# Kernel tuning notes

Hardware: AMD Instinct MI355X
Metric: run time of the kernel (lower is better)

## Reference

```python
import jax, jax.numpy as jnp
import numpy as np

N = 50000      # nodes
E = 800000     # edges (before self-loops)
IN = 128       # in_channels
HID = 64       # hidden_channels
HEADS = 4      # num_heads of gat1
ACT = 5        # num_actions
NEG_SLOPE = 0.2


def gat_conv(x, edge_index, W, a_src, a_dst, bias, heads, out_ch):
    """PyG-style GATConv (concat=True, add_self_loops=True, eval mode)."""
    n = x.shape[0]
    loops = jnp.arange(n)
    src = jnp.concatenate([edge_index[0], loops])  # messages flow src -> dst
    dst = jnp.concatenate([edge_index[1], loops])
    h = (x @ W).reshape(n, heads, out_ch)                 # [N,H,C]
    alpha_src = jnp.sum(h * a_src, axis=-1)               # [N,H]
    alpha_dst = jnp.sum(h * a_dst, axis=-1)               # [N,H]
    e = jax.nn.leaky_relu(alpha_src[src] + alpha_dst[dst], NEG_SLOPE)  # [Et,H]
    # numerically-stable segment softmax over incoming edges of each dst node
    e_max = jax.lax.stop_gradient(jax.ops.segment_max(e, dst, num_segments=n))
    e_max = jnp.where(jnp.isfinite(e_max), e_max, 0.0)
    p = jnp.exp(e - e_max[dst])                           # [Et,H]
    denom = jax.ops.segment_sum(p, dst, num_segments=n)   # [N,H]
    alpha = p / (denom[dst] + 1e-16)                      # [Et,H]
    out = jax.ops.segment_sum(h[src] * alpha[:, :, None], dst, num_segments=n)
    return out.reshape(n, heads * out_ch) + bias


def setup_inputs() -> dict:
    key = jax.random.key(0)
    ks = jax.random.split(key, 12)
    s = 0.1
    return {
        "x": jax.random.normal(ks[0], (N, IN), jnp.float32),
        "edge_index": jax.random.randint(ks[1], (2, E), 0, N, dtype=jnp.int32),
        "W1": jax.random.normal(ks[2], (IN, HEADS * HID), jnp.float32) * s,
        "a1_src": jax.random.normal(ks[3], (HEADS, HID), jnp.float32) * s,
        "a1_dst": jax.random.normal(ks[4], (HEADS, HID), jnp.float32) * s,
        "b1": jnp.zeros((HEADS * HID,), jnp.float32),
        "W2": jax.random.normal(ks[5], (HEADS * HID, HID), jnp.float32) * s,
        "a2_src": jax.random.normal(ks[6], (1, HID), jnp.float32) * s,
        "a2_dst": jax.random.normal(ks[7], (1, HID), jnp.float32) * s,
        "b2": jnp.zeros((HID,), jnp.float32),
        "Wfc": jax.random.normal(ks[8], (HID, ACT), jnp.float32) * s,
        "bfc": jnp.zeros((ACT,), jnp.float32),
    }


def reference(x, edge_index, W1, a1_src, a1_dst, b1, W2, a2_src, a2_dst, b2, Wfc, bfc):
    # x.view(-1, F) is a no-op for already-flat [N, F] input; dropout skipped (eval).
    h = jax.nn.relu(gat_conv(x, edge_index, W1, a1_src, a1_dst, b1, HEADS, HID))
    h = jax.nn.relu(gat_conv(h, edge_index, W2, a2_src, a2_dst, b2, 1, HID))
    return h @ Wfc + bfc  # [N, num_actions]
```

## Files before the change

### kernel.cpp

```cpp
#include <hip/hip_runtime.h>

#define NEG_SLOPE 0.2f

__device__ __forceinline__ float leaky(float x) { return x > 0.f ? x : NEG_SLOPE * x; }

__global__ void k_count(const int* __restrict__ dst, int E, int* __restrict__ cnt) {
    int i = blockIdx.x * blockDim.x + threadIdx.x;
    if (i < E) atomicAdd(&cnt[dst[i]], 1);
}

__global__ __launch_bounds__(256) void k_scanA(const int* __restrict__ cnt, int* __restrict__ rowptr,
                                               int* __restrict__ bsum, int n) {
    int b = blockIdx.x, t = threadIdx.x;
    int lane = t & 63, w = t >> 6;
    int i0 = b * 1024 + t * 4;
    int v0 = (i0 + 0 < n) ? cnt[i0 + 0] : 0;
    int v1 = (i0 + 1 < n) ? cnt[i0 + 1] : 0;
    int v2 = (i0 + 2 < n) ? cnt[i0 + 2] : 0;
    int v3 = (i0 + 3 < n) ? cnt[i0 + 3] : 0;
    int r0 = v0, r1 = r0 + v1, r2 = r1 + v2, r3 = r2 + v3;
    int s = r3;
    int q = s;
    #pragma unroll
    for (int off = 1; off < 64; off <<= 1) {
        int tval = __shfl_up(q, off);
        if (lane >= off) q += tval;
    }
    __shared__ int wsum[4];
    if (lane == 63) wsum[w] = q;
    __syncthreads();
    int woff = 0;
    #pragma unroll
    for (int k = 0; k < 4; k++) if (k < w) woff += wsum[k];
    int excl = woff + q - s;
    if (i0 + 0 < n) rowptr[1 + i0 + 0] = excl + r0;
    if (i0 + 1 < n) rowptr[1 + i0 + 1] = excl + r1;
    if (i0 + 2 < n) rowptr[1 + i0 + 2] = excl + r2;
    if (i0 + 3 < n) rowptr[1 + i0 + 3] = excl + r3;
    if (t == 255) bsum[b] = woff + q;
}

__global__ void k_scanB(const int* __restrict__ bsum, int* __restrict__ bscan, int nb) {
    int lane = threadIdx.x & 63;
    int v = (lane < nb) ? bsum[lane] : 0;
    #pragma unroll
    for (int off = 1; off < 64; off <<= 1) {
        int t = __shfl_up(v, off);
        if (lane >= off) v += t;
    }
    if (lane < nb) bscan[lane] = v;
}

__global__ __launch_bounds__(256) void k_scanC(int* __restrict__ rowptr, const int* __restrict__ bscan, int n) {
    int b = blockIdx.x, t = threadIdx.x;
    int i0 = b * 1024 + t * 4;
    if (b == 0) {
        if (t == 0) rowptr[0] = 0;
        return;
    }
    int add = bscan[b - 1];
    #pragma unroll
    for (int j = 0; j < 4; j++)
        if (i0 + j < n) rowptr[1 + i0 + j] += add;
}

__global__ void k_copy(const int* __restrict__ src, int* __restrict__ dst, int n) {
    int i = blockIdx.x * blockDim.x + threadIdx.x;
    if (i < n) dst[i] = src[i];
}

__global__ void k_scatter(const int* __restrict__ srcn, const int* __restrict__ dstn, int E,
                          int* __restrict__ wptr, int* __restrict__ col) {
    int i = blockIdx.x * blockDim.x + threadIdx.x;
    if (i < E) {
        int d = dstn[i];
        int pos = atomicAdd(&wptr[d], 1);
        col[pos] = srcn[i];
    }
}

template <int BMT>
__global__ __launch_bounds__(256) void k_gemm(const float* __restrict__ A, const float* __restrict__ B,
                                              float* __restrict__ C, int M, int N, int K) {
    constexpr int RT = BMT / 16;
    constexpr int APASS = BMT / 32;
    __shared__ float As[32][BMT + 4];
    __shared__ float Bs[32][68];
    int row0 = blockIdx.x * BMT, col0 = blockIdx.y * 64;
    int tid = threadIdx.x;
    int tx = tid & 15, ty = tid >> 4;
    float acc[RT][4] = {};
    for (int kk = 0; kk < K; kk += 32) {
        int ar = tid >> 3;
        int ac = (tid & 7) * 4;
        #pragma unroll
        for (int p = 0; p < APASS; p++) {
            int r = ar + p * 32;
            int gr = row0 + r;
            float4 v = make_float4(0.f, 0.f, 0.f, 0.f);
            if (gr < M) v = *reinterpret_cast<const float4*>(&A[(size_t)gr * K + kk + ac]);
            As[ac + 0][r] = v.x; As[ac + 1][r] = v.y;
            As[ac + 2][r] = v.z; As[ac + 3][r] = v.w;
        }
        int br = tid >> 4;
        int bc = (tid & 15) * 4;
        #pragma unroll
        for (int p = 0; p < 2; p++) {
            int r = br + p * 16;
            float4 v = *reinterpret_cast<const float4*>(&B[(size_t)(kk + r) * N + col0 + bc]);
            *reinterpret_cast<float4*>(&Bs[r][bc]) = v;
        }
        __syncthreads();
        #pragma unroll
        for (int k = 0; k < 32; k++) {
            float a[RT];
            #pragma unroll
            for (int i = 0; i < RT; i += 4) {
                float4 av = *reinterpret_cast<const float4*>(&As[k][ty * RT + i]);
                a[i + 0] = av.x; a[i + 1] = av.y; a[i + 2] = av.z; a[i + 3] = av.w;
            }
            float4 bv = *reinterpret_cast<const float4*>(&Bs[k][tx * 4]);
            float b[4] = {bv.x, bv.y, bv.z, bv.w};
            #pragma unroll
            for (int i = 0; i < RT; i++)
                #pragma unroll
                for (int j = 0; j < 4; j++) acc[i][j] = fmaf(a[i], b[j], acc[i][j]);
        }
        __syncthreads();
    }
    #pragma unroll
    for (int i = 0; i < RT; i++) {
        int gr = row0 + ty * RT + i;
        if (gr < M) {
            float4 v = make_float4(acc[i][0], acc[i][1], acc[i][2], acc[i][3]);
            *reinterpret_cast<float4*>(&C[(size_t)gr * N + col0 + tx * 4]) = v;
        }
    }
}

__global__ __launch_bounds__(256) void k_alpha1(const float* __restrict__ h,
                                                const float* __restrict__ a_s, const float* __restrict__ a_d,
                                                float* __restrict__ asrc, float* __restrict__ adst, int n) {
    int node = blockIdx.x;
    int t = threadIdx.x, hd = t >> 6, lane = t & 63;
    float v = h[(size_t)node * 256 + t];
    float ps = v * a_s[t], pd = v * a_d[t];
    #pragma unroll
    for (int off = 32; off; off >>= 1) { ps += __shfl_xor(ps, off); pd += __shfl_xor(pd, off); }
    if (lane == 0) { asrc[node * 4 + hd] = ps; adst[node * 4 + hd] = pd; }
}

__global__ __launch_bounds__(256) void k_alpha2(const float* __restrict__ h,
                                                const float* __restrict__ a_s, const float* __restrict__ a_d,
                                                float* __restrict__ asrc, float* __restrict__ adst, int n) {
    int node = blockIdx.x * 4 + (threadIdx.x >> 6);
    int lane = threadIdx.x & 63;
    if (node >= n) return;
    float v = h[(size_t)node * 64 + lane];
    float ps = v * a_s[lane], pd = v * a_d[lane];
    #pragma unroll
    for (int off = 32; off; off >>= 1) { ps += __shfl_xor(ps, off); pd += __shfl_xor(pd, off); }
    if (lane == 0) { asrc[node] = ps; adst[node] = pd; }
}

__global__ __launch_bounds__(256) void k_agg1(const float* __restrict__ h, const float* __restrict__ asrc,
                                              const float* __restrict__ adst, const int* __restrict__ rowptr,
                                              const int* __restrict__ col, const float* __restrict__ bias,
                                              float* __restrict__ out, int n) {
    int node = blockIdx.x;
    int t = threadIdx.x, hd = t >> 6, l = t & 63;
    int rep = l >> 4, q = l & 15;
    int base = rowptr[node], deg = rowptr[node + 1] - base;
    float adst_n = adst[node * 4 + hd];
    float e_self = leaky(asrc[node * 4 + hd] + adst_n);
    float m = e_self;
    for (int i = l; i < deg; i += 64) {
        int s = col[base + i];
        m = fmaxf(m, leaky(asrc[s * 4 + hd] + adst_n));
    }
    #pragma unroll
    for (int off = 32; off; off >>= 1) m = fmaxf(m, __shfl_xor(m, off));

    float p_self = __expf(e_self - m);
    float4 acc = make_float4(0.f, 0.f, 0.f, 0.f);
    if (rep == 0) {
        float4 hv = *reinterpret_cast<const float4*>(&h[(size_t)node * 256 + hd * 64 + q * 4]);
        acc.x = p_self * hv.x; acc.y = p_self * hv.y; acc.z = p_self * hv.z; acc.w = p_self * hv.w;
    }
    float dsum = (l == 0) ? p_self : 0.f;

    for (int c0 = 0; c0 < deg; c0 += 8) {
        int ia = c0 + rep, ib = ia + 4;
        bool va = ia < deg, vb = ib < deg;
        int sa = 0, sb = 0;
        if (va) sa = col[base + ia];
        if (vb) sb = col[base + ib];
        float4 ha = make_float4(0.f, 0.f, 0.f, 0.f), hb = ha;
        if (va) ha = *reinterpret_cast<const float4*>(&h[(size_t)sa * 256 + hd * 64 + q * 4]);
        if (vb) hb = *reinterpret_cast<const float4*>(&h[(size_t)sb * 256 + hd * 64 + q * 4]);
        float pa = 0.f, pb = 0.f;
        if (va) pa = __expf(leaky(asrc[sa * 4 + hd] + adst_n) - m);
        if (vb) pb = __expf(leaky(asrc[sb * 4 + hd] + adst_n) - m);
        acc.x = fmaf(pa, ha.x, acc.x); acc.y = fmaf(pa, ha.y, acc.y);
        acc.z = fmaf(pa, ha.z, acc.z); acc.w = fmaf(pa, ha.w, acc.w);
        acc.x = fmaf(pb, hb.x, acc.x); acc.y = fmaf(pb, hb.y, acc.y);
        acc.z = fmaf(pb, hb.z, acc.z); acc.w = fmaf(pb, hb.w, acc.w);
        if (q == 0) dsum += pa + pb;
    }
    #pragma unroll
    for (int off = 16; off <= 32; off <<= 1) {
        acc.x += __shfl_xor(acc.x, off); acc.y += __shfl_xor(acc.y, off);
        acc.z += __shfl_xor(acc.z, off); acc.w += __shfl_xor(acc.w, off);
    }
    #pragma unroll
    for (int off = 32; off; off >>= 1) dsum += __shfl_xor(dsum, off);
    if (rep == 0) {
        float inv = 1.f / (dsum + 1e-16f);
        float4 bv = *reinterpret_cast<const float4*>(&bias[hd * 64 + q * 4]);
        float4 r;
        r.x = fmaxf(acc.x * inv + bv.x, 0.f);
        r.y = fmaxf(acc.y * inv + bv.y, 0.f);
        r.z = fmaxf(acc.z * inv + bv.z, 0.f);
        r.w = fmaxf(acc.w * inv + bv.w, 0.f);
        *reinterpret_cast<float4*>(&out[(size_t)node * 256 + hd * 64 + q * 4]) = r;
    }
}

__global__ __launch_bounds__(256) void k_agg2fc(const float* __restrict__ h, const float* __restrict__ asrc,
                                                const float* __restrict__ adst, const int* __restrict__ rowptr,
                                                const int* __restrict__ col, const float* __restrict__ bias,
                                                const float* __restrict__ Wfc, const float* __restrict__ bfc,
                                                float* __restrict__ out, int n) {
    int node = blockIdx.x * 4 + (threadIdx.x >> 6);
    int l = threadIdx.x & 63;
    if (node >= n) return;
    int rep = l >> 4, q = l & 15;
    int base = rowptr[node], deg = rowptr[node + 1] - base;
    float adst_n = adst[node];
    float e_self = leaky(asrc[node] + adst_n);
    float m = e_self;
    for (int i = l; i < deg; i += 64) {
        int s = col[base + i];
        m = fmaxf(m, leaky(asrc[s] + adst_n));
    }
    #pragma unroll
    for (int off = 32; off; off >>= 1) m = fmaxf(m, __shfl_xor(m, off));

    float p_self = __expf(e_self - m);
    float4 acc = make_float4(0.f, 0.f, 0.f, 0.f);
    if (rep == 0) {
        float4 hv = *reinterpret_cast<const float4*>(&h[(size_t)node * 64 + q * 4]);
        acc.x = p_self * hv.x; acc.y = p_self * hv.y; acc.z = p_self * hv.z; acc.w = p_self * hv.w;
    }
    float dsum = (l == 0) ? p_self : 0.f;

    for (int c0 = 0; c0 < deg; c0 += 8) {
        int ia = c0 + rep, ib = ia + 4;
        bool va = ia < deg, vb = ib < deg;
        int sa = 0, sb = 0;
        if (va) sa = col[base + ia];
        if (vb) sb = col[base + ib];
        float4 ha = make_float4(0.f, 0.f, 0.f, 0.f), hb = ha;
        if (va) ha = *reinterpret_cast<const float4*>(&h[(size_t)sa * 64 + q * 4]);
        if (vb) hb = *reinterpret_cast<const float4*>(&h[(size_t)sb * 64 + q * 4]);
        float pa = 0.f, pb = 0.f;
        if (va) pa = __expf(leaky(asrc[sa] + adst_n) - m);
        if (vb) pb = __expf(leaky(asrc[sb] + adst_n) - m);
        acc.x = fmaf(pa, ha.x, acc.x); acc.y = fmaf(pa, ha.y, acc.y);
        acc.z = fmaf(pa, ha.z, acc.z); acc.w = fmaf(pa, ha.w, acc.w);
        acc.x = fmaf(pb, hb.x, acc.x); acc.y = fmaf(pb, hb.y, acc.y);
        acc.z = fmaf(pb, hb.z, acc.z); acc.w = fmaf(pb, hb.w, acc.w);
        if (q == 0) dsum += pa + pb;
    }
    #pragma unroll
    for (int off = 16; off <= 32; off <<= 1) {
        acc.x += __shfl_xor(acc.x, off); acc.y += __shfl_xor(acc.y, off);
        acc.z += __shfl_xor(acc.z, off); acc.w += __shfl_xor(acc.w, off);
    }
    #pragma unroll
    for (int off = 32; off; off >>= 1) dsum += __shfl_xor(dsum, off);
    float inv = 1.f / (dsum + 1e-16f);
    float r0 = fmaxf(acc.x * inv + bias[q * 4 + 0], 0.f);
    float r1 = fmaxf(acc.y * inv + bias[q * 4 + 1], 0.f);
    float r2 = fmaxf(acc.z * inv + bias[q * 4 + 2], 0.f);
    float r3 = fmaxf(acc.w * inv + bias[q * 4 + 3], 0.f);
    #pragma unroll
    for (int a = 0; a < 5; a++) {
        float part = r0 * Wfc[(q * 4 + 0) * 5 + a] + r1 * Wfc[(q * 4 + 1) * 5 + a]
                   + r2 * Wfc[(q * 4 + 2) * 5 + a] + r3 * Wfc[(q * 4 + 3) * 5 + a];
        #pragma unroll
        for (int off = 1; off <= 8; off <<= 1) part += __shfl_xor(part, off);
        if (l == 0) out[(size_t)node * 5 + a] = part + bfc[a];
    }
}

extern "C" void kernel_launch(void* const* d_in, const int* in_sizes, int n_in,
                              void* d_out, int out_size, void* d_ws, size_t ws_size,
                              hipStream_t stream) {
    const float* x   = (const float*)d_in[0];
    const int*   ei  = (const int*)d_in[1];
    const float* W1  = (const float*)d_in[2];
    const float* a1s = (const float*)d_in[3];
    const float* a1d = (const float*)d_in[4];
    const float* b1  = (const float*)d_in[5];
    const float* W2  = (const float*)d_in[6];
    const float* a2s = (const float*)d_in[7];
    const float* a2d = (const float*)d_in[8];
    const float* b2  = (const float*)d_in[9];
    const float* Wfc = (const float*)d_in[10];
    const float* bfc = (const float*)d_in[11];
    float* out = (float*)d_out;

    int n = in_sizes[0] / 128;
    int E = in_sizes[1] / 2;
    const int* srcn = ei;
    const int* dstn = ei + E;

    char* ws = (char*)d_ws;
    size_t off = 0;
    auto alloc = [&](size_t bytes) -> void* {
        void* p = ws + off;
        off += (bytes + 255) & ~(size_t)255;
        return p;
    };
    float* h1     = (float*)alloc((size_t)n * 256 * 4);
    float* out1   = (float*)alloc((size_t)n * 256 * 4);
    float* asrc1  = (float*)alloc((size_t)n * 4 * 4);
    float* adst1  = (float*)alloc((size_t)n * 4 * 4);
    int*   rowptr = (int*)alloc((size_t)(n + 1) * 4);
    int*   wptr   = (int*)alloc((size_t)n * 4);
    int*   col    = (int*)alloc((size_t)E * 4);
    int*   bsum   = (int*)alloc(64 * 4);
    int*   bscan  = (int*)alloc(64 * 4);
    float* h2    = h1;
    float* asrc2 = asrc1;
    float* adst2 = adst1;

    int nb = (n + 1023) / 1024;

    hipMemsetAsync(wptr, 0, (size_t)n * 4, stream);
    k_count<<<(E + 255) / 256, 256, 0, stream>>>(dstn, E, wptr);
    k_scanA<<<nb, 256, 0, stream>>>(wptr, rowptr, bsum, n);
    k_scanB<<<1, 64, 0, stream>>>(bsum, bscan, nb);
    k_scanC<<<nb, 256, 0, stream>>>(rowptr, bscan, n);
    k_copy<<<(n + 255) / 256, 256, 0, stream>>>(rowptr, wptr, n);
    k_scatter<<<(E + 255) / 256, 256, 0, stream>>>(srcn, dstn, E, wptr, col);

    k_gemm<128><<<dim3((n + 127) / 128, 4), 256, 0, stream>>>(x, W1, h1, n, 256, 128);
    k_alpha1<<<n, 256, 0, stream>>>(h1, a1s, a1d, asrc1, adst1, n);
    k_agg1<<<n, 256, 0, stream>>>(h1, asrc1, adst1, rowptr, col, b1, out1, n);
    k_gemm<64><<<dim3((n + 63) / 64, 1), 256, 0, stream>>>(out1, W2, h2, n, 64, 256);
    k_alpha2<<<(n + 3) / 4, 256, 0, stream>>>(h2, a2s, a2d, asrc2, adst2, n);
    k_agg2fc<<<(n + 3) / 4, 256, 0, stream>>>(h2, asrc2, adst2, rowptr, col, b2, Wfc, bfc, out, n);
}
```

Baseline: 546.5 us.

## Fuse attention logits into GEMM epilogue and store layer-1 features as bf16

The GEMM epilogue now computes per-head source and destination attention dot products with a 16-lane shuffle reduction, which removes the separate alpha kernels and their re-read of h. Layer-1 projected features are written only as bf16, so the gather-heavy aggregation kernel reads half as many bytes per neighbour, with each lane handling 8 channels and 8 neighbours processed in parallel. This trades precision in the aggregated features for lower memory traffic. The attention logits are still computed from the fp32 accumulators.

```diff
diff --git a/kernel.cpp b/kernel.cpp
--- a/kernel.cpp
+++ b/kernel.cpp
@@ -3,6 +3,18 @@
 #define NEG_SLOPE 0.2f
 
 __device__ __forceinline__ float leaky(float x) { return x > 0.f ? x : NEG_SLOPE * x; }
+
+__device__ __forceinline__ void unpack2(unsigned u, float& lo, float& hi) {
+    union { unsigned u; float f; } a, b;
+    a.u = u << 16; b.u = u & 0xffff0000u;
+    lo = a.f; hi = b.f;
+}
+
+__device__ __forceinline__ unsigned short f2bf(float f) {
+    unsigned u = __float_as_uint(f);
+    u += 0x7fffu + ((u >> 16) & 1u);
+    return (unsigned short)(u >> 16);
+}
 
 __global__ void k_count(const int* __restrict__ dst, int E, int* __restrict__ cnt) {
     int i = blockIdx.x * blockDim.x + threadIdx.x;
@@ -79,9 +91,12 @@
     }
 }
 
-template <int BMT>
+template <int BMT, bool WF32, bool WBF16, bool FALPHA>
 __global__ __launch_bounds__(256) void k_gemm(const float* __restrict__ A, const float* __restrict__ B,
-                                              float* __restrict__ C, int M, int N, int K) {
+                                              float* __restrict__ C, unsigned short* __restrict__ Cb,
+                                              const float* __restrict__ a_s, const float* __restrict__ a_d,
+                                              float* __restrict__ asrc, float* __restrict__ adst,
+                                              int M, int N, int K) {
     constexpr int RT = BMT / 16;
     constexpr int APASS = BMT / 32;
     __shared__ float As[32][BMT + 4];
@@ -128,48 +143,44 @@
         }
         __syncthreads();
     }
+    float4 as4, ad4;
+    if (FALPHA) {
+        as4 = *reinterpret_cast<const float4*>(&a_s[col0 + tx * 4]);
+        ad4 = *reinterpret_cast<const float4*>(&a_d[col0 + tx * 4]);
+    }
+    int HV = N >> 6, hd = col0 >> 6;
     #pragma unroll
     for (int i = 0; i < RT; i++) {
         int gr = row0 + ty * RT + i;
         if (gr < M) {
-            float4 v = make_float4(acc[i][0], acc[i][1], acc[i][2], acc[i][3]);
-            *reinterpret_cast<float4*>(&C[(size_t)gr * N + col0 + tx * 4]) = v;
+            if (WF32) {
+                float4 v = make_float4(acc[i][0], acc[i][1], acc[i][2], acc[i][3]);
+                *reinterpret_cast<float4*>(&C[(size_t)gr * N + col0 + tx * 4]) = v;
+            }
+            if (WBF16) {
+                ushort4 u;
+                u.x = f2bf(acc[i][0]); u.y = f2bf(acc[i][1]);
+                u.z = f2bf(acc[i][2]); u.w = f2bf(acc[i][3]);
+                *reinterpret_cast<ushort4*>(&Cb[(size_t)gr * N + col0 + tx * 4]) = u;
+            }
+            if (FALPHA) {
+                float ps = acc[i][0] * as4.x + acc[i][1] * as4.y + acc[i][2] * as4.z + acc[i][3] * as4.w;
+                float pd = acc[i][0] * ad4.x + acc[i][1] * ad4.y + acc[i][2] * ad4.z + acc[i][3] * ad4.w;
+                #pragma unroll
+                for (int off = 1; off <= 8; off <<= 1) { ps += __shfl_xor(ps, off); pd += __shfl_xor(pd, off); }
+                if (tx == 0) { asrc[(size_t)gr * HV + hd] = ps; adst[(size_t)gr * HV + hd] = pd; }
+            }
         }
     }
 }
 
-__global__ __launch_bounds__(256) void k_alpha1(const float* __restrict__ h,
-                                                const float* __restrict__ a_s, const float* __restrict__ a_d,
-                                                float* __restrict__ asrc, float* __restrict__ adst, int n) {
-    int node = blockIdx.x;
-    int t = threadIdx.x, hd = t >> 6, lane = t & 63;
-    float v = h[(size_t)node * 256 + t];
-    float ps = v * a_s[t], pd = v * a_d[t];
-    #pragma unroll
-    for (int off = 32; off; off >>= 1) { ps += __shfl_xor(ps, off); pd += __shfl_xor(pd, off); }
-    if (lane == 0) { asrc[node * 4 + hd] = ps; adst[node * 4 + hd] = pd; }
-}
-
-__global__ __launch_bounds__(256) void k_alpha2(const float* __restrict__ h,
-                                                const float* __restrict__ a_s, const float* __restrict__ a_d,
-                                                float* __restrict__ asrc, float* __restrict__ adst, int n) {
-    int node = blockIdx.x * 4 + (threadIdx.x >> 6);
-    int lane = threadIdx.x & 63;
-    if (node >= n) return;
-    float v = h[(size_t)node * 64 + lane];
-    float ps = v * a_s[lane], pd = v * a_d[lane];
-    #pragma unroll
-    for (int off = 32; off; off >>= 1) { ps += __shfl_xor(ps, off); pd += __shfl_xor(pd, off); }
-    if (lane == 0) { asrc[node] = ps; adst[node] = pd; }
-}
-
-__global__ __launch_bounds__(256) void k_agg1(const float* __restrict__ h, const float* __restrict__ asrc,
-                                              const float* __restrict__ adst, const int* __restrict__ rowptr,
-                                              const int* __restrict__ col, const float* __restrict__ bias,
-                                              float* __restrict__ out, int n) {
+__global__ __launch_bounds__(256) void k_agg1(const unsigned short* __restrict__ hb,
+                                              const float* __restrict__ asrc, const float* __restrict__ adst,
+                                              const int* __restrict__ rowptr, const int* __restrict__ col,
+                                              const float* __restrict__ bias, float* __restrict__ out, int n) {
     int node = blockIdx.x;
     int t = threadIdx.x, hd = t >> 6, l = t & 63;
-    int rep = l >> 4, q = l & 15;
+    int rep = l >> 3, q = l & 7;
     int base = rowptr[node], deg = rowptr[node + 1] - base;
     float adst_n = adst[node * 4 + hd];
     float e_self = leaky(asrc[node * 4 + hd] + adst_n);
@@ -182,47 +193,55 @@
     for (int off = 32; off; off >>= 1) m = fmaxf(m, __shfl_xor(m, off));
 
     float p_self = __expf(e_self - m);
-    float4 acc = make_float4(0.f, 0.f, 0.f, 0.f);
+    float acc[8] = {};
     if (rep == 0) {
-        float4 hv = *reinterpret_cast<const float4*>(&h[(size_t)node * 256 + hd * 64 + q * 4]);
-        acc.x = p_self * hv.x; acc.y = p_self * hv.y; acc.z = p_self * hv.z; acc.w = p_self * hv.w;
+        uint4 u = *reinterpret_cast<const uint4*>(&hb[(size_t)node * 256 + hd * 64 + q * 8]);
+        float f[8];
+        unpack2(u.x, f[0], f[1]); unpack2(u.y, f[2], f[3]);
+        unpack2(u.z, f[4], f[5]); unpack2(u.w, f[6], f[7]);
+        #pragma unroll
+        for (int j = 0; j < 8; j++) acc[j] = p_self * f[j];
     }
     float dsum = (l == 0) ? p_self : 0.f;
 
-    for (int c0 = 0; c0 < deg; c0 += 8) {
-        int ia = c0 + rep, ib = ia + 4;
+    for (int c0 = 0; c0 < deg; c0 += 16) {
+        int ia = c0 + rep, ib = ia + 8;
         bool va = ia < deg, vb = ib < deg;
         int sa = 0, sb = 0;
         if (va) sa = col[base + ia];
         if (vb) sb = col[base + ib];
-        float4 ha = make_float4(0.f, 0.f, 0.f, 0.f), hb = ha;
-        if (va) ha = *reinterpret_cast<const float4*>(&h[(size_t)sa * 256 + hd * 64 + q * 4]);
-        if (vb) hb = *reinterpret_cast<const float4*>(&h[(size_t)sb * 256 + hd * 64 + q * 4]);
+        uint4 ua = make_uint4(0, 0, 0, 0), ub = make_uint4(0, 0, 0, 0);
+        if (va) ua = *reinterpret_cast<const uint4*>(&hb[(size_t)sa * 256 + hd * 64 + q * 8]);
+        if (vb) ub = *reinterpret_cast<const uint4*>(&hb[(size_t)sb * 256 + hd * 64 + q * 8]);
         float pa = 0.f, pb = 0.f;
         if (va) pa = __expf(leaky(asrc[sa * 4 + hd] + adst_n) - m);
         if (vb) pb = __expf(leaky(asrc[sb * 4 + hd] + adst_n) - m);
-        acc.x = fmaf(pa, ha.x, acc.x); acc.y = fmaf(pa, ha.y, acc.y);
-        acc.z = fmaf(pa, ha.z, acc.z); acc.w = fmaf(pa, ha.w, acc.w);
-        acc.x = fmaf(pb, hb.x, acc.x); acc.y = fmaf(pb, hb.y, acc.y);
-        acc.z = fmaf(pb, hb.z, acc.z); acc.w = fmaf(pb, hb.w, acc.w);
+        float f[8];
+        unpack2(ua.x, f[0], f[1]); unpack2(ua.y, f[2], f[3]);
+        unpack2(ua.z, f[4], f[5]); unpack2(ua.w, f[6], f[7]);
+        #pragma unroll
+        for (int j = 0; j < 8; j++) acc[j] = fmaf(pa, f[j], acc[j]);
+        unpack2(ub.x, f[0], f[1]); unpack2(ub.y, f[2], f[3]);
+        unpack2(ub.z, f[4], f[5]); unpack2(ub.w, f[6], f[7]);
+        #pragma unroll
+        for (int j = 0; j < 8; j++) acc[j] = fmaf(pb, f[j], acc[j]);
         if (q == 0) dsum += pa + pb;
     }
     #pragma unroll
-    for (int off = 16; off <= 32; off <<= 1) {
-        acc.x += __shfl_xor(acc.x, off); acc.y += __shfl_xor(acc.y, off);
-        acc.z += __shfl_xor(acc.z, off); acc.w += __shfl_xor(acc.w, off);
-    }
+    for (int off = 8; off <= 32; off <<= 1)
+        #pragma unroll
+        for (int j = 0; j < 8; j++) acc[j] += __shfl_xor(acc[j], off);
     #pragma unroll
     for (int off = 32; off; off >>= 1) dsum += __shfl_xor(dsum, off);
     if (rep == 0) {
         float inv = 1.f / (dsum + 1e-16f);
-        float4 bv = *reinterpret_cast<const float4*>(&bias[hd * 64 + q * 4]);
-        float4 r;
-        r.x = fmaxf(acc.x * inv + bv.x, 0.f);
-        r.y = fmaxf(acc.y * inv + bv.y, 0.f);
-        r.z = fmaxf(acc.z * inv + bv.z, 0.f);
-        r.w = fmaxf(acc.w * inv + bv.w, 0.f);
-        *reinterpret_cast<float4*>(&out[(size_t)node * 256 + hd * 64 + q * 4]) = r;
+        float r[8];
+        #pragma unroll
+        for (int j = 0; j < 8; j++) r[j] = fmaxf(acc[j] * inv + bias[hd * 64 + q * 8 + j], 0.f);
+        float4 v0 = make_float4(r[0], r[1], r[2], r[3]);
+        float4 v1 = make_float4(r[4], r[5], r[6], r[7]);
+        *reinterpret_cast<float4*>(&out[(size_t)node * 256 + hd * 64 + q * 8]) = v0;
+        *reinterpret_cast<float4*>(&out[(size_t)node * 256 + hd * 64 + q * 8 + 4]) = v1;
     }
 }
 
@@ -260,16 +279,16 @@
         int sa = 0, sb = 0;
         if (va) sa = col[base + ia];
         if (vb) sb = col[base + ib];
-        float4 ha = make_float4(0.f, 0.f, 0.f, 0.f), hb = ha;
+        float4 ha = make_float4(0.f, 0.f, 0.f, 0.f), hbv = ha;
         if (va) ha = *reinterpret_cast<const float4*>(&h[(size_t)sa * 64 + q * 4]);
-        if (vb) hb = *reinterpret_cast<const float4*>(&h[(size_t)sb * 64 + q * 4]);
+        if (vb) hbv = *reinterpret_cast<const float4*>(&h[(size_t)sb * 64 + q * 4]);
         float pa = 0.f, pb = 0.f;
         if (va) pa = __expf(leaky(asrc[sa] + adst_n) - m);
         if (vb) pb = __expf(leaky(asrc[sb] + adst_n) - m);
         acc.x = fmaf(pa, ha.x, acc.x); acc.y = fmaf(pa, ha.y, acc.y);
         acc.z = fmaf(pa, ha.z, acc.z); acc.w = fmaf(pa, ha.w, acc.w);
-        acc.x = fmaf(pb, hb.x, acc.x); acc.y = fmaf(pb, hb.y, acc.y);
-        acc.z = fmaf(pb, hb.z, acc.z); acc.w = fmaf(pb, hb.w, acc.w);
+        acc.x = fmaf(pb, hbv.x, acc.x); acc.y = fmaf(pb, hbv.y, acc.y);
+        acc.z = fmaf(pb, hbv.z, acc.z); acc.w = fmaf(pb, hbv.w, acc.w);
         if (q == 0) dsum += pa + pb;
     }
     #pragma unroll
@@ -323,8 +342,9 @@
         off += (bytes + 255) & ~(size_t)255;
         return p;
     };
-    float* h1     = (float*)alloc((size_t)n * 256 * 4);
+    unsigned short* h1b = (unsigned short*)alloc((size_t)n * 256 * 2);
     float* out1   = (float*)alloc((size_t)n * 256 * 4);
+    float* h2     = (float*)alloc((size_t)n * 64 * 4);
     float* asrc1  = (float*)alloc((size_t)n * 4 * 4);
     float* adst1  = (float*)alloc((size_t)n * 4 * 4);
     int*   rowptr = (int*)alloc((size_t)(n + 1) * 4);
@@ -332,7 +352,6 @@
     int*   col    = (int*)alloc((size_t)E * 4);
     int*   bsum   = (int*)alloc(64 * 4);
     int*   bscan  = (int*)alloc(64 * 4);
-    float* h2    = h1;
     float* asrc2 = asrc1;
     float* adst2 = adst1;
 
@@ -346,10 +365,10 @@
     k_copy<<<(n + 255) / 256, 256, 0, stream>>>(rowptr, wptr, n);
     k_scatter<<<(E + 255) / 256, 256, 0, stream>>>(srcn, dstn, E, wptr, col);
 
-    k_gemm<128><<<dim3((n + 127) / 128, 4), 256, 0, stream>>>(x, W1, h1, n, 256, 128);
-    k_alpha1<<<n, 256, 0, stream>>>(h1, a1s, a1d, asrc1, adst1, n);
-    k_agg1<<<n, 256, 0, stream>>>(h1, asrc1, adst1, rowptr, col, b1, out1, n);
-    k_gemm<64><<<dim3((n + 63) / 64, 1), 256, 0, stream>>>(out1, W2, h2, n, 64, 256);
-    k_alpha2<<<(n + 3) / 4, 256, 0, stream>>>(h2, a2s, a2d, asrc2, adst2, n);
+    k_gemm<128, false, true, true><<<dim3((n + 127) / 128, 4), 256, 0, stream>>>(
+        x, W1, nullptr, h1b, a1s, a1d, asrc1, adst1, n, 256, 128);
+    k_agg1<<<n, 256, 0, stream>>>(h1b, asrc1, adst1, rowptr, col, b1, out1, n);
+    k_gemm<64, true, false, true><<<dim3((n + 63) / 64, 1), 256, 0, stream>>>(
+        out1, W2, h2, nullptr, a2s, a2d, asrc2, adst2, n, 64, 256);
     k_agg2fc<<<(n + 3) / 4, 256, 0, stream>>>(h2, asrc2, adst2, rowptr, col, b2, Wfc, bfc, out, n);
 }
```

Measured after the change: 489.0 us. -10.5%, faster.
